# Optimization experiments

Measured on AMD Instinct MI355X. Metric: run time of the kernel, lower is better.

## Reference

```python
import jax, jax.numpy as jnp
import numpy as np

N, S, Z, H, K, DEG = 8192, 4, 64, 128, 4, 16
E = N * DEG


def setup_inputs() -> dict:
    key = jax.random.key(0)
    ks = jax.random.split(key, 9)
    g = lambda k, shape, scale=1.0: jax.random.normal(k, shape, dtype=jnp.float32) * scale
    return dict(
        zIG=g(ks[0], (N, S, Z)),                         # node intention features
        xt_enc=g(ks[1], (N, S, H)),                      # encoded actions per node
        Ws=g(ks[2], (K, H, Z), 1.0 / np.sqrt(Z)),        # attn_s[k] weights (no bias)
        Wd=g(ks[3], (K, H, Z), 1.0 / np.sqrt(Z)),        # attn_d[k] weights
        F2_w1=g(ks[4], (H, 2 * H), 1.0 / np.sqrt(2 * H)),
        F2_w2=g(ks[5], (H, H), 1.0 / np.sqrt(H)),
        F1_w1=g(ks[6], (H, K * H), 1.0 / np.sqrt(K * H)),
        F1_w2=g(ks[7], (H, H), 1.0 / np.sqrt(H)),
        src=jax.random.randint(ks[8], (E,), 0, N),       # random source per edge
        dst=jnp.repeat(jnp.arange(N), DEG),              # regular graph: DEG in-edges per node, grouped
    )


def reference(zIG, xt_enc, Ws, Wd, F2_w1, F2_w2, F1_w1, F1_w2, src, dst):
    n, s, h = xt_enc.shape
    k = Ws.shape[0]
    deg = src.shape[0] // n

    # ---- edge_attention: eIG[e,s,k] = leaky_relu(sum_h (Ws_k z_src)*(Wd_k z_dst)) ----
    zs, zd = zIG[src], zIG[dst]                          # [E,S,Z] irregular gathers
    scores = []
    for kk in range(k):                                  # k is small & structural
        a_s = zs @ Ws[kk].T                              # [E,S,H]
        a_d = zd @ Wd[kk].T                              # [E,S,H]
        scores.append(jax.nn.leaky_relu((a_s * a_d).sum(-1)))  # [E,S]
    eIG = jnp.stack(scores, axis=-1)                     # [E,S,K]

    # ---- message_func: dA = F2(cat(xt_src, xt_dst)) ----
    msg_in = jnp.concatenate([xt_enc[src], xt_enc[dst]], axis=-1)   # [E,S,2H]
    dA = jax.nn.relu(msg_in @ F2_w1.T) @ F2_w2.T                    # [E,S,H]

    # ---- reduce_func: softmax over neighbor mailbox (dim=1), weighted mean ----
    # dst is grouped with constant degree, so the DGL mailbox is a reshape.
    alpha = jax.nn.softmax(eIG.reshape(n, deg, s, k), axis=1)       # [N,D,S,K]
    mail = dA.reshape(n, deg, s, h)                                 # [N,D,S,H]
    res = jnp.einsum('ndsk,ndsh->nskh', alpha, mail) / deg          # mean over D
    res = res.reshape(n, s, k * h)                                  # cat over k (k-major)
    deltax = jax.nn.relu(res @ F1_w1.T) @ F1_w2.T                   # [N,S,H]
    return deltax, alpha
```

## Files before the change

### kernel.cpp

```cpp
#include <hip/hip_runtime.h>
#include <hip/hip_bf16.h>

typedef unsigned short u16;
using ushort8 = __attribute__((ext_vector_type(8))) unsigned short;
using short8  = __attribute__((ext_vector_type(8))) short;
using f32x4   = __attribute__((ext_vector_type(4))) float;

__device__ __forceinline__ float bf2f(u16 v) {
  union { unsigned int u; float f; } x; x.u = ((unsigned int)v) << 16; return x.f;
}
__device__ __forceinline__ u16 f2bf(float f) {
  union { unsigned int u; float f; } x; x.f = f;
  unsigned int r = x.u + 0x7FFFu + ((x.u >> 16) & 1u);
  return (u16)(r >> 16);
}
__device__ __forceinline__ float dot4(float4 a, float4 b) {
  return a.x * b.x + a.y * b.y + a.z * b.z + a.w * b.w;
}
__device__ __forceinline__ void stage_w(const float* g, int stride, int c, u16* Wl, int t) {
  int row = t >> 1, half = t & 1;
  const float4* gp = (const float4*)(g + (size_t)row * stride + c * 64 + half * 32);
  ushort8* d = (ushort8*)(Wl + row * 72 + half * 32);
  #pragma unroll
  for (int i = 0; i < 4; ++i) {
    float4 a = gp[2 * i], b = gp[2 * i + 1];
    ushort8 o;
    o[0] = f2bf(a.x); o[1] = f2bf(a.y); o[2] = f2bf(a.z); o[3] = f2bf(a.w);
    o[4] = f2bf(b.x); o[5] = f2bf(b.y); o[6] = f2bf(b.z); o[7] = f2bf(b.w);
    d[i] = o;
  }
}

__global__ __launch_bounds__(256) void k_mt(const float* __restrict__ Ws,
                                            const float* __restrict__ Wd,
                                            float* __restrict__ MT) {
  int t = blockIdx.x * 256 + threadIdx.x;
  int k = t >> 12, z2 = (t >> 6) & 63, z1 = t & 63;
  const float* wsp = Ws + k * 8192 + z1;
  const float* wdp = Wd + k * 8192 + z2;
  float acc = 0.f;
  #pragma unroll 8
  for (int h = 0; h < 128; ++h) acc += wsp[h * 64] * wdp[h * 64];
  MT[k * 4096 + z2 * 64 + z1] = acc;
}

__global__ __launch_bounds__(256) void k_td(const float* __restrict__ zIG,
                                            const float* __restrict__ MT,
                                            float* __restrict__ td) {
  __shared__ float zf[8 * 256];
  int t = threadIdx.x;
  int nb0 = blockIdx.x * 8;
  {
    const float4* zsrc = (const float4*)(zIG + (size_t)nb0 * 256);
    float4* zd = (float4*)zf;
    zd[t] = zsrc[t];
    zd[t + 256] = zsrc[t + 256];
  }
  __syncthreads();
  int s = t >> 6, k = (t >> 4) & 3, z1q = t & 15;
  const float4* mt4 = (const float4*)MT;
  float4 acc[8];
  #pragma unroll
  for (int g = 0; g < 8; ++g) acc[g] = make_float4(0.f, 0.f, 0.f, 0.f);
  for (int z2 = 0; z2 < 64; ++z2) {
    float4 mv = mt4[k * 1024 + z2 * 16 + z1q];
    #pragma unroll
    for (int g = 0; g < 8; ++g) {
      float zv = zf[g * 256 + s * 64 + z2];
      acc[g].x += mv.x * zv; acc[g].y += mv.y * zv;
      acc[g].z += mv.z * zv; acc[g].w += mv.w * zv;
    }
  }
  int sk = s * 4 + k;
  #pragma unroll
  for (int g = 0; g < 8; ++g)
    *(float4*)&td[(size_t)(nb0 + g) * 1024 + sk * 64 + z1q * 4] = acc[g];
}

__global__ __launch_bounds__(256) void k_ww(const float* __restrict__ F1w1,
                                            const float* __restrict__ F2w2,
                                            float* __restrict__ WW2) {
  int id = blockIdx.x * 256 + threadIdx.x;
  int ho = id >> 9, kk = (id >> 7) & 3, hi = id & 127;
  const float* wa = F1w1 + ho * 512 + kk * 128;
  const float* wb = F2w2 + hi;
  float acc = 0.f;
  #pragma unroll 8
  for (int j = 0; j < 128; ++j) acc += wa[j] * wb[j * 128];
  WW2[ho * 512 + kk * 128 + hi] = acc * 0.0625f;
}

__global__ __launch_bounds__(256) void k_uv(const float* __restrict__ xt,
                                            const float* __restrict__ W1,
                                            u16* __restrict__ u, u16* __restrict__ v) {
  __shared__ u16 Wlu[128 * 72];
  __shared__ u16 Wlv[128 * 72];
  int t = threadIdx.x, lane = t & 63, w = t >> 6;
  size_t rowbase = (size_t)blockIdx.x * 128 + w * 32;
  int l15 = lane & 15, kc = lane >> 4;
  f32x4 au[2][8], av[2][8];
  #pragma unroll
  for (int mt = 0; mt < 2; ++mt)
    #pragma unroll
    for (int nt = 0; nt < 8; ++nt) {
      au[mt][nt] = (f32x4){0.f, 0.f, 0.f, 0.f};
      av[mt][nt] = (f32x4){0.f, 0.f, 0.f, 0.f};
    }
  for (int c = 0; c < 2; ++c) {
    __syncthreads();
    stage_w(W1,       256, c, Wlu, t);
    stage_w(W1 + 128, 256, c, Wlv, t);
    __syncthreads();
    #pragma unroll
    for (int ks = 0; ks < 2; ++ks) {
      short8 af[2];
      #pragma unroll
      for (int mt = 0; mt < 2; ++mt) {
        const float* ap = xt + (rowbase + mt * 16 + l15) * 128 + c * 64 + ks * 32 + kc * 8;
        float4 a0 = *(const float4*)ap, a1 = *(const float4*)(ap + 4);
        u16 tmp[8] = {f2bf(a0.x), f2bf(a0.y), f2bf(a0.z), f2bf(a0.w),
                      f2bf(a1.x), f2bf(a1.y), f2bf(a1.z), f2bf(a1.w)};
        af[mt] = *(short8*)tmp;
      }
      #pragma unroll
      for (int nt = 0; nt < 8; ++nt) {
        short8 bu = *(const short8*)&Wlu[(nt * 16 + l15) * 72 + ks * 32 + kc * 8];
        short8 bv = *(const short8*)&Wlv[(nt * 16 + l15) * 72 + ks * 32 + kc * 8];
        #pragma unroll
        for (int mt = 0; mt < 2; ++mt) {
          au[mt][nt] = __builtin_amdgcn_mfma_f32_16x16x32_bf16(af[mt], bu, au[mt][nt], 0, 0, 0);
          av[mt][nt] = __builtin_amdgcn_mfma_f32_16x16x32_bf16(af[mt], bv, av[mt][nt], 0, 0, 0);
        }
      }
    }
  }
  #pragma unroll
  for (int mt = 0; mt < 2; ++mt)
    #pragma unroll
    for (int nt = 0; nt < 8; ++nt)
      #pragma unroll
      for (int j = 0; j < 4; ++j) {
        size_t idx = (rowbase + mt * 16 + kc * 4 + j) * 128 + nt * 16 + l15;
        u[idx] = f2bf(au[mt][nt][j]);
        v[idx] = f2bf(av[mt][nt][j]);
      }
}

__global__ __launch_bounds__(256) void k_score(
    const float* __restrict__ zIG, const int* __restrict__ src,
    const float* __restrict__ td, const u16* __restrict__ uW, const u16* __restrict__ vW,
    float* __restrict__ out, u16* __restrict__ m_ws) {
  __shared__ int srcIdx[16];
  __shared__ float tds[16 * 68];
  __shared__ float sc[16 * 17];
  __shared__ float al[16 * 17];
  __shared__ float vn[512];

  int t = threadIdx.x, n = blockIdx.x;
  if (t < 16) srcIdx[t] = src[n * 16 + t];
  {
    int r = t >> 4, cc = t & 15;
    *(float4*)&tds[r * 68 + cc * 4] = ((const float4*)(td + (size_t)n * 1024))[r * 16 + cc];
  }
  if (t < 128) ((float4*)vn)[t] = make_float4(bf2f(vW[(size_t)n * 512 + t * 4]),
                                              bf2f(vW[(size_t)n * 512 + t * 4 + 1]),
                                              bf2f(vW[(size_t)n * 512 + t * 4 + 2]),
                                              bf2f(vW[(size_t)n * 512 + t * 4 + 3]));
  __syncthreads();
  {
    int d = t >> 4, s = (t >> 2) & 3, k = t & 3;
    int sn = srcIdx[d];
    const float4* zp = (const float4*)(zIG + (size_t)sn * 256 + s * 64);
    const float4* ta = (const float4*)&tds[(s * 4 + k) * 68];
    float acc = 0.f;
    #pragma unroll
    for (int z4 = 0; z4 < 16; ++z4) acc += dot4(zp[z4], ta[z4]);
    sc[d * 17 + s * 4 + k] = acc > 0.f ? acc : 0.01f * acc;
  }
  __syncthreads();
  {
    int d = t >> 4, sk = t & 15;
    float mx = -3.4e38f;
    #pragma unroll
    for (int dd = 0; dd < 16; ++dd) mx = fmaxf(mx, sc[dd * 17 + sk]);
    float sum = 0.f, eown = 0.f;
    #pragma unroll
    for (int dd = 0; dd < 16; ++dd) {
      float e = __expf(sc[dd * 17 + sk] - mx);
      sum += e;
      if (dd == d) eown = e;
    }
    float a = eown / sum;
    al[d * 17 + sk] = a;
    out[4194304u + (unsigned)n * 256 + t] = a;
  }
  __syncthreads();
  {
    int h = t & 127, s0 = t >> 7;
    float mac[2][4] = {{0.f,0.f,0.f,0.f},{0.f,0.f,0.f,0.f}};
    for (int d = 0; d < 16; ++d) {
      int sn = srcIdx[d];
      #pragma unroll
      for (int pi = 0; pi < 2; ++pi) {
        int s = s0 + pi * 2;
        float uval = bf2f(uW[(size_t)sn * 512 + s * 128 + h]) + vn[s * 128 + h];
        float hid = uval > 0.f ? uval : 0.f;
        #pragma unroll
        for (int k = 0; k < 4; ++k) mac[pi][k] += al[d * 17 + s * 4 + k] * hid;
      }
    }
    #pragma unroll
    for (int pi = 0; pi < 2; ++pi) {
      int s = s0 + pi * 2;
      #pragma unroll
      for (int k = 0; k < 4; ++k)
        m_ws[(size_t)n * 2048 + (s * 4 + k) * 128 + h] = f2bf(mac[pi][k]);
    }
  }
}

__global__ __launch_bounds__(256) void k_fg(const u16* __restrict__ A,
                                            const float* __restrict__ WF,
                                            const float* __restrict__ WG,
                                            float* __restrict__ out) {
  __shared__ u16 Wl[128 * 72];
  __shared__ u16 hidl[128 * 136];
  int t = threadIdx.x, lane = t & 63, w = t >> 6;
  size_t rowbase = (size_t)blockIdx.x * 128 + w * 32;
  int l15 = lane & 15, kc = lane >> 4;
  f32x4 acc[2][8];
  #pragma unroll
  for (int mt = 0; mt < 2; ++mt)
    #pragma unroll
    for (int nt = 0; nt < 8; ++nt) acc[mt][nt] = (f32x4){0.f, 0.f, 0.f, 0.f};
  for (int c = 0; c < 8; ++c) {
    __syncthreads();
    stage_w(WF, 512, c, Wl, t);
    __syncthreads();
    #pragma unroll
    for (int ks = 0; ks < 2; ++ks) {
      short8 af[2];
      #pragma unroll
      for (int mt = 0; mt < 2; ++mt)
        af[mt] = *(const short8*)(A + (rowbase + mt * 16 + l15) * 512 + c * 64 + ks * 32 + kc * 8);
      #pragma unroll
      for (int nt = 0; nt < 8; ++nt) {
        short8 bf = *(const short8*)&Wl[(nt * 16 + l15) * 72 + ks * 32 + kc * 8];
        #pragma unroll
        for (int mt = 0; mt < 2; ++mt)
          acc[mt][nt] = __builtin_amdgcn_mfma_f32_16x16x32_bf16(af[mt], bf, acc[mt][nt], 0, 0, 0);
      }
    }
  }
  #pragma unroll
  for (int mt = 0; mt < 2; ++mt)
    #pragma unroll
    for (int nt = 0; nt < 8; ++nt)
      #pragma unroll
      for (int j = 0; j < 4; ++j)
        hidl[(w * 32 + mt * 16 + kc * 4 + j) * 136 + nt * 16 + l15] =
            f2bf(fmaxf(acc[mt][nt][j], 0.f));
  f32x4 acc2[2][8];
  #pragma unroll
  for (int mt = 0; mt < 2; ++mt)
    #pragma unroll
    for (int nt = 0; nt < 8; ++nt) acc2[mt][nt] = (f32x4){0.f, 0.f, 0.f, 0.f};
  for (int c = 0; c < 2; ++c) {
    __syncthreads();
    stage_w(WG, 128, c, Wl, t);
    __syncthreads();
    #pragma unroll
    for (int ks = 0; ks < 2; ++ks) {
      short8 af[2];
      #pragma unroll
      for (int mt = 0; mt < 2; ++mt)
        af[mt] = *(const short8*)&hidl[(w * 32 + mt * 16 + l15) * 136 + c * 64 + ks * 32 + kc * 8];
      #pragma unroll
      for (int nt = 0; nt < 8; ++nt) {
        short8 bf = *(const short8*)&Wl[(nt * 16 + l15) * 72 + ks * 32 + kc * 8];
        #pragma unroll
        for (int mt = 0; mt < 2; ++mt)
          acc2[mt][nt] = __builtin_amdgcn_mfma_f32_16x16x32_bf16(af[mt], bf, acc2[mt][nt], 0, 0, 0);
      }
    }
  }
  #pragma unroll
  for (int mt = 0; mt < 2; ++mt)
    #pragma unroll
    for (int nt = 0; nt < 8; ++nt)
      #pragma unroll
      for (int j = 0; j < 4; ++j)
        out[(rowbase + mt * 16 + kc * 4 + j) * 128 + nt * 16 + l15] = acc2[mt][nt][j];
}

extern "C" void kernel_launch(void* const* d_in, const int* in_sizes, int n_in,
                              void* d_out, int out_size, void* d_ws, size_t ws_size,
                              hipStream_t stream) {
  const float* zIG  = (const float*)d_in[0];
  const float* xt   = (const float*)d_in[1];
  const float* Ws   = (const float*)d_in[2];
  const float* Wd   = (const float*)d_in[3];
  const float* F2w1 = (const float*)d_in[4];
  const float* F2w2 = (const float*)d_in[5];
  const float* F1w1 = (const float*)d_in[6];
  const float* F1w2 = (const float*)d_in[7];
  const int* src    = (const int*)d_in[8];
  float* out = (float*)d_out;

  char* ws = (char*)d_ws;
  float* MT  = (float*)ws;
  float* td  = (float*)(ws + 65536);
  u16* u     = (u16*)(ws + 65536 + 33554432);
  u16* v     = u + 4194304;
  float* WW2 = (float*)(ws + 50397184);
  u16* m     = (u16*)(ws + 50659328);

  k_mt   <<<64,   256, 0, stream>>>(Ws, Wd, MT);
  k_td   <<<1024, 256, 0, stream>>>(zIG, MT, td);
  k_ww   <<<256,  256, 0, stream>>>(F1w1, F2w2, WW2);
  k_uv   <<<256,  256, 0, stream>>>(xt, F2w1, u, v);
  k_score<<<8192, 256, 0, stream>>>(zIG, src, td, u, v, out, m);
  k_fg   <<<256,  256, 0, stream>>>(m, WW2, F1w2, out);
}
```

Before: 122.5 us.

## Merge independent prep kernels and vectorize score kernel gathers and softmax

Folds k_mt and k_ww into one launch, and k_td and k_uv into a second launch that dispatches on block index, cutting six launches to four and letting independent work overlap. In k_score the per-edge score dot products now have each lane load a quarter of z and reduce through wave shuffles. The softmax is split into separate max/exp and sum phases with an added barrier. The message accumulation reads u and v as packed bf16 pairs, with two h values per thread, and writes packed outputs. These changes aim to cut launch gaps and memory transactions, at the cost of a larger merged kernel with shared-memory use set by its biggest branch, and an extra sync.

```diff
diff --git a/kernel.cpp b/kernel.cpp
--- a/kernel.cpp
+++ b/kernel.cpp
@@ -2,17 +2,24 @@
 #include <hip/hip_bf16.h>
 
 typedef unsigned short u16;
+typedef unsigned int u32;
 using ushort8 = __attribute__((ext_vector_type(8))) unsigned short;
 using short8  = __attribute__((ext_vector_type(8))) short;
 using f32x4   = __attribute__((ext_vector_type(4))) float;
 
 __device__ __forceinline__ float bf2f(u16 v) {
-  union { unsigned int u; float f; } x; x.u = ((unsigned int)v) << 16; return x.f;
+  union { u32 u; float f; } x; x.u = ((u32)v) << 16; return x.f;
+}
+__device__ __forceinline__ float u2f(u32 u) {
+  union { u32 u; float f; } x; x.u = u; return x.f;
 }
 __device__ __forceinline__ u16 f2bf(float f) {
-  union { unsigned int u; float f; } x; x.f = f;
-  unsigned int r = x.u + 0x7FFFu + ((x.u >> 16) & 1u);
+  union { u32 u; float f; } x; x.f = f;
+  u32 r = x.u + 0x7FFFu + ((x.u >> 16) & 1u);
   return (u16)(r >> 16);
+}
+__device__ __forceinline__ u32 pack2bf(float lo, float hi) {
+  return (u32)f2bf(lo) | ((u32)f2bf(hi) << 16);
 }
 __device__ __forceinline__ float dot4(float4 a, float4 b) {
   return a.x * b.x + a.y * b.y + a.z * b.z + a.w * b.w;
@@ -31,119 +38,122 @@
   }
 }
 
-__global__ __launch_bounds__(256) void k_mt(const float* __restrict__ Ws,
-                                            const float* __restrict__ Wd,
-                                            float* __restrict__ MT) {
-  int t = blockIdx.x * 256 + threadIdx.x;
-  int k = t >> 12, z2 = (t >> 6) & 63, z1 = t & 63;
-  const float* wsp = Ws + k * 8192 + z1;
-  const float* wdp = Wd + k * 8192 + z2;
-  float acc = 0.f;
-  #pragma unroll 8
-  for (int h = 0; h < 128; ++h) acc += wsp[h * 64] * wdp[h * 64];
-  MT[k * 4096 + z2 * 64 + z1] = acc;
-}
-
-__global__ __launch_bounds__(256) void k_td(const float* __restrict__ zIG,
-                                            const float* __restrict__ MT,
-                                            float* __restrict__ td) {
-  __shared__ float zf[8 * 256];
+__global__ __launch_bounds__(256) void k_prep(const float* __restrict__ Ws,
+                                              const float* __restrict__ Wd,
+                                              const float* __restrict__ F1w1,
+                                              const float* __restrict__ F2w2,
+                                              float* __restrict__ MT,
+                                              float* __restrict__ WW2) {
+  if (blockIdx.x < 64) {
+    int t = blockIdx.x * 256 + threadIdx.x;
+    int k = t >> 12, z2 = (t >> 6) & 63, z1 = t & 63;
+    const float* wsp = Ws + k * 8192 + z1;
+    const float* wdp = Wd + k * 8192 + z2;
+    float acc = 0.f;
+    #pragma unroll 8
+    for (int h = 0; h < 128; ++h) acc += wsp[h * 64] * wdp[h * 64];
+    MT[k * 4096 + z2 * 64 + z1] = acc;
+  } else {
+    int id = (blockIdx.x - 64) * 256 + threadIdx.x;
+    int ho = id >> 9, kk = (id >> 7) & 3, hi = id & 127;
+    const float* wa = F1w1 + ho * 512 + kk * 128;
+    const float* wb = F2w2 + hi;
+    float acc = 0.f;
+    #pragma unroll 8
+    for (int j = 0; j < 128; ++j) acc += wa[j] * wb[j * 128];
+    WW2[ho * 512 + kk * 128 + hi] = acc * 0.0625f;
+  }
+}
+
+__global__ __launch_bounds__(256) void k_stage2(const float* __restrict__ zIG,
+                                                const float* __restrict__ MT,
+                                                const float* __restrict__ xt,
+                                                const float* __restrict__ W1,
+                                                float* __restrict__ td,
+                                                u16* __restrict__ u, u16* __restrict__ v) {
+  __shared__ __align__(16) char smem[36864];
   int t = threadIdx.x;
-  int nb0 = blockIdx.x * 8;
-  {
-    const float4* zsrc = (const float4*)(zIG + (size_t)nb0 * 256);
-    float4* zd = (float4*)zf;
-    zd[t] = zsrc[t];
-    zd[t + 256] = zsrc[t + 256];
-  }
-  __syncthreads();
-  int s = t >> 6, k = (t >> 4) & 3, z1q = t & 15;
-  const float4* mt4 = (const float4*)MT;
-  float4 acc[8];
-  #pragma unroll
-  for (int g = 0; g < 8; ++g) acc[g] = make_float4(0.f, 0.f, 0.f, 0.f);
-  for (int z2 = 0; z2 < 64; ++z2) {
-    float4 mv = mt4[k * 1024 + z2 * 16 + z1q];
-    #pragma unroll
-    for (int g = 0; g < 8; ++g) {
-      float zv = zf[g * 256 + s * 64 + z2];
-      acc[g].x += mv.x * zv; acc[g].y += mv.y * zv;
-      acc[g].z += mv.z * zv; acc[g].w += mv.w * zv;
-    }
-  }
-  int sk = s * 4 + k;
-  #pragma unroll
-  for (int g = 0; g < 8; ++g)
-    *(float4*)&td[(size_t)(nb0 + g) * 1024 + sk * 64 + z1q * 4] = acc[g];
-}
-
-__global__ __launch_bounds__(256) void k_ww(const float* __restrict__ F1w1,
-                                            const float* __restrict__ F2w2,
-                                            float* __restrict__ WW2) {
-  int id = blockIdx.x * 256 + threadIdx.x;
-  int ho = id >> 9, kk = (id >> 7) & 3, hi = id & 127;
-  const float* wa = F1w1 + ho * 512 + kk * 128;
-  const float* wb = F2w2 + hi;
-  float acc = 0.f;
-  #pragma unroll 8
-  for (int j = 0; j < 128; ++j) acc += wa[j] * wb[j * 128];
-  WW2[ho * 512 + kk * 128 + hi] = acc * 0.0625f;
-}
-
-__global__ __launch_bounds__(256) void k_uv(const float* __restrict__ xt,
-                                            const float* __restrict__ W1,
-                                            u16* __restrict__ u, u16* __restrict__ v) {
-  __shared__ u16 Wlu[128 * 72];
-  __shared__ u16 Wlv[128 * 72];
-  int t = threadIdx.x, lane = t & 63, w = t >> 6;
-  size_t rowbase = (size_t)blockIdx.x * 128 + w * 32;
-  int l15 = lane & 15, kc = lane >> 4;
-  f32x4 au[2][8], av[2][8];
-  #pragma unroll
-  for (int mt = 0; mt < 2; ++mt)
-    #pragma unroll
-    for (int nt = 0; nt < 8; ++nt) {
-      au[mt][nt] = (f32x4){0.f, 0.f, 0.f, 0.f};
-      av[mt][nt] = (f32x4){0.f, 0.f, 0.f, 0.f};
-    }
-  for (int c = 0; c < 2; ++c) {
-    __syncthreads();
-    stage_w(W1,       256, c, Wlu, t);
-    stage_w(W1 + 128, 256, c, Wlv, t);
-    __syncthreads();
-    #pragma unroll
-    for (int ks = 0; ks < 2; ++ks) {
-      short8 af[2];
-      #pragma unroll
-      for (int mt = 0; mt < 2; ++mt) {
-        const float* ap = xt + (rowbase + mt * 16 + l15) * 128 + c * 64 + ks * 32 + kc * 8;
-        float4 a0 = *(const float4*)ap, a1 = *(const float4*)(ap + 4);
-        u16 tmp[8] = {f2bf(a0.x), f2bf(a0.y), f2bf(a0.z), f2bf(a0.w),
-                      f2bf(a1.x), f2bf(a1.y), f2bf(a1.z), f2bf(a1.w)};
-        af[mt] = *(short8*)tmp;
-      }
+  if (blockIdx.x < 1024) {
+    float* zf = (float*)smem;
+    int nb0 = blockIdx.x * 8;
+    {
+      const float4* zsrc = (const float4*)(zIG + (size_t)nb0 * 256);
+      float4* zd = (float4*)zf;
+      zd[t] = zsrc[t];
+      zd[t + 256] = zsrc[t + 256];
+    }
+    __syncthreads();
+    int s = t >> 6, k = (t >> 4) & 3, z1q = t & 15;
+    const float4* mt4 = (const float4*)MT;
+    float4 acc[8];
+    #pragma unroll
+    for (int g = 0; g < 8; ++g) acc[g] = make_float4(0.f, 0.f, 0.f, 0.f);
+    for (int z2 = 0; z2 < 64; ++z2) {
+      float4 mv = mt4[k * 1024 + z2 * 16 + z1q];
+      #pragma unroll
+      for (int g = 0; g < 8; ++g) {
+        float zv = zf[g * 256 + s * 64 + z2];
+        acc[g].x += mv.x * zv; acc[g].y += mv.y * zv;
+        acc[g].z += mv.z * zv; acc[g].w += mv.w * zv;
+      }
+    }
+    int sk = s * 4 + k;
+    #pragma unroll
+    for (int g = 0; g < 8; ++g)
+      *(float4*)&td[(size_t)(nb0 + g) * 1024 + sk * 64 + z1q * 4] = acc[g];
+  } else {
+    u16* Wlu = (u16*)smem;
+    u16* Wlv = (u16*)(smem + 18432);
+    int lane = t & 63, w = t >> 6;
+    size_t rowbase = (size_t)(blockIdx.x - 1024) * 128 + w * 32;
+    int l15 = lane & 15, kc = lane >> 4;
+    f32x4 au[2][8], av[2][8];
+    #pragma unroll
+    for (int mt = 0; mt < 2; ++mt)
       #pragma unroll
       for (int nt = 0; nt < 8; ++nt) {
-        short8 bu = *(const short8*)&Wlu[(nt * 16 + l15) * 72 + ks * 32 + kc * 8];
-        short8 bv = *(const short8*)&Wlv[(nt * 16 + l15) * 72 + ks * 32 + kc * 8];
+        au[mt][nt] = (f32x4){0.f, 0.f, 0.f, 0.f};
+        av[mt][nt] = (f32x4){0.f, 0.f, 0.f, 0.f};
+      }
+    for (int c = 0; c < 2; ++c) {
+      __syncthreads();
+      stage_w(W1,       256, c, Wlu, t);
+      stage_w(W1 + 128, 256, c, Wlv, t);
+      __syncthreads();
+      #pragma unroll
+      for (int ks = 0; ks < 2; ++ks) {
+        short8 af[2];
         #pragma unroll
         for (int mt = 0; mt < 2; ++mt) {
-          au[mt][nt] = __builtin_amdgcn_mfma_f32_16x16x32_bf16(af[mt], bu, au[mt][nt], 0, 0, 0);
-          av[mt][nt] = __builtin_amdgcn_mfma_f32_16x16x32_bf16(af[mt], bv, av[mt][nt], 0, 0, 0);
+          const float* ap = xt + (rowbase + mt * 16 + l15) * 128 + c * 64 + ks * 32 + kc * 8;
+          float4 a0 = *(const float4*)ap, a1 = *(const float4*)(ap + 4);
+          u16 tmp[8] = {f2bf(a0.x), f2bf(a0.y), f2bf(a0.z), f2bf(a0.w),
+                        f2bf(a1.x), f2bf(a1.y), f2bf(a1.z), f2bf(a1.w)};
+          af[mt] = *(short8*)tmp;
         }
-      }
-    }
-  }
-  #pragma unroll
-  for (int mt = 0; mt < 2; ++mt)
-    #pragma unroll
-    for (int nt = 0; nt < 8; ++nt)
-      #pragma unroll
-      for (int j = 0; j < 4; ++j) {
-        size_t idx = (rowbase + mt * 16 + kc * 4 + j) * 128 + nt * 16 + l15;
-        u[idx] = f2bf(au[mt][nt][j]);
-        v[idx] = f2bf(av[mt][nt][j]);
-      }
+        #pragma unroll
+        for (int nt = 0; nt < 8; ++nt) {
+          short8 bu = *(const short8*)&Wlu[(nt * 16 + l15) * 72 + ks * 32 + kc * 8];
+          short8 bv = *(const short8*)&Wlv[(nt * 16 + l15) * 72 + ks * 32 + kc * 8];
+          #pragma unroll
+          for (int mt = 0; mt < 2; ++mt) {
+            au[mt][nt] = __builtin_amdgcn_mfma_f32_16x16x32_bf16(af[mt], bu, au[mt][nt], 0, 0, 0);
+            av[mt][nt] = __builtin_amdgcn_mfma_f32_16x16x32_bf16(af[mt], bv, av[mt][nt], 0, 0, 0);
+          }
+        }
+      }
+    }
+    #pragma unroll
+    for (int mt = 0; mt < 2; ++mt)
+      #pragma unroll
+      for (int nt = 0; nt < 8; ++nt)
+        #pragma unroll
+        for (int j = 0; j < 4; ++j) {
+          size_t idx = (rowbase + mt * 16 + kc * 4 + j) * 128 + nt * 16 + l15;
+          u[idx] = f2bf(au[mt][nt][j]);
+          v[idx] = f2bf(av[mt][nt][j]);
+        }
+  }
 }
 
 __global__ __launch_bounds__(256) void k_score(
@@ -152,9 +162,9 @@
     float* __restrict__ out, u16* __restrict__ m_ws) {
   __shared__ int srcIdx[16];
   __shared__ float tds[16 * 68];
-  __shared__ float sc[16 * 17];
-  __shared__ float al[16 * 17];
-  __shared__ float vn[512];
+  __shared__ float s17[16 * 17];
+  __shared__ float e17[16 * 17];
+  __shared__ float a20[16 * 20];
 
   int t = threadIdx.x, n = blockIdx.x;
   if (t < 16) srcIdx[t] = src[n * 16 + t];
@@ -162,60 +172,72 @@
     int r = t >> 4, cc = t & 15;
     *(float4*)&tds[r * 68 + cc * 4] = ((const float4*)(td + (size_t)n * 1024))[r * 16 + cc];
   }
-  if (t < 128) ((float4*)vn)[t] = make_float4(bf2f(vW[(size_t)n * 512 + t * 4]),
-                                              bf2f(vW[(size_t)n * 512 + t * 4 + 1]),
-                                              bf2f(vW[(size_t)n * 512 + t * 4 + 2]),
-                                              bf2f(vW[(size_t)n * 512 + t * 4 + 3]));
   __syncthreads();
   {
     int d = t >> 4, s = (t >> 2) & 3, k = t & 3;
     int sn = srcIdx[d];
     const float4* zp = (const float4*)(zIG + (size_t)sn * 256 + s * 64);
-    const float4* ta = (const float4*)&tds[(s * 4 + k) * 68];
-    float acc = 0.f;
-    #pragma unroll
-    for (int z4 = 0; z4 < 16; ++z4) acc += dot4(zp[z4], ta[z4]);
-    sc[d * 17 + s * 4 + k] = acc > 0.f ? acc : 0.01f * acc;
+    int base = s * 4;
+    float p0 = 0.f, p1 = 0.f, p2 = 0.f, p3 = 0.f;
+    #pragma unroll
+    for (int i = 0; i < 4; ++i) {
+      float4 zv = zp[i * 4 + k];
+      int o = i * 16 + k * 4;
+      p0 += dot4(zv, *(const float4*)&tds[(base + 0) * 68 + o]);
+      p1 += dot4(zv, *(const float4*)&tds[(base + 1) * 68 + o]);
+      p2 += dot4(zv, *(const float4*)&tds[(base + 2) * 68 + o]);
+      p3 += dot4(zv, *(const float4*)&tds[(base + 3) * 68 + o]);
+    }
+    p0 += __shfl_xor(p0, 1); p1 += __shfl_xor(p1, 1);
+    p2 += __shfl_xor(p2, 1); p3 += __shfl_xor(p3, 1);
+    p0 += __shfl_xor(p0, 2); p1 += __shfl_xor(p1, 2);
+    p2 += __shfl_xor(p2, 2); p3 += __shfl_xor(p3, 2);
+    float acc = (k == 0) ? p0 : (k == 1) ? p1 : (k == 2) ? p2 : p3;
+    s17[d * 17 + base + k] = acc > 0.f ? acc : 0.01f * acc;
   }
   __syncthreads();
-  {
-    int d = t >> 4, sk = t & 15;
+  float e_own;
+  int dC = t >> 4, skC = t & 15;
+  {
     float mx = -3.4e38f;
     #pragma unroll
-    for (int dd = 0; dd < 16; ++dd) mx = fmaxf(mx, sc[dd * 17 + sk]);
-    float sum = 0.f, eown = 0.f;
-    #pragma unroll
-    for (int dd = 0; dd < 16; ++dd) {
-      float e = __expf(sc[dd * 17 + sk] - mx);
-      sum += e;
-      if (dd == d) eown = e;
-    }
-    float a = eown / sum;
-    al[d * 17 + sk] = a;
+    for (int dd = 0; dd < 16; ++dd) mx = fmaxf(mx, s17[dd * 17 + skC]);
+    e_own = __expf(s17[dC * 17 + skC] - mx);
+    e17[dC * 17 + skC] = e_own;
+  }
+  __syncthreads();
+  {
+    float sum = 0.f;
+    #pragma unroll
+    for (int dd = 0; dd < 16; ++dd) sum += e17[dd * 17 + skC];
+    float a = e_own / sum;
+    a20[dC * 20 + skC] = a;
     out[4194304u + (unsigned)n * 256 + t] = a;
   }
   __syncthreads();
   {
-    int h = t & 127, s0 = t >> 7;
-    float mac[2][4] = {{0.f,0.f,0.f,0.f},{0.f,0.f,0.f,0.f}};
+    int hp = t & 63, s = t >> 6;
+    u32 vbits = *(const u32*)(vW + (size_t)n * 512 + s * 128 + hp * 2);
+    float v_lo = u2f(vbits << 16), v_hi = u2f(vbits & 0xffff0000u);
+    const u32* up = (const u32*)uW;
+    float m0l = 0.f, m0h = 0.f, m1l = 0.f, m1h = 0.f;
+    float m2l = 0.f, m2h = 0.f, m3l = 0.f, m3h = 0.f;
     for (int d = 0; d < 16; ++d) {
       int sn = srcIdx[d];
-      #pragma unroll
-      for (int pi = 0; pi < 2; ++pi) {
-        int s = s0 + pi * 2;
-        float uval = bf2f(uW[(size_t)sn * 512 + s * 128 + h]) + vn[s * 128 + h];
-        float hid = uval > 0.f ? uval : 0.f;
-        #pragma unroll
-        for (int k = 0; k < 4; ++k) mac[pi][k] += al[d * 17 + s * 4 + k] * hid;
-      }
-    }
-    #pragma unroll
-    for (int pi = 0; pi < 2; ++pi) {
-      int s = s0 + pi * 2;
-      #pragma unroll
-      for (int k = 0; k < 4; ++k)
-        m_ws[(size_t)n * 2048 + (s * 4 + k) * 128 + h] = f2bf(mac[pi][k]);
-    }
+      u32 ub = up[(size_t)sn * 256 + s * 64 + hp];
+      float r_lo = fmaxf(u2f(ub << 16) + v_lo, 0.f);
+      float r_hi = fmaxf(u2f(ub & 0xffff0000u) + v_hi, 0.f);
+      float4 a = *(const float4*)&a20[d * 20 + s * 4];
+      m0l += a.x * r_lo; m0h += a.x * r_hi;
+      m1l += a.y * r_lo; m1h += a.y * r_hi;
+      m2l += a.z * r_lo; m2h += a.z * r_hi;
+      m3l += a.w * r_lo; m3h += a.w * r_hi;
+    }
+    u32* mp = (u32*)(m_ws + (size_t)n * 2048);
+    mp[(s * 4 + 0) * 64 + hp] = pack2bf(m0l, m0h);
+    mp[(s * 4 + 1) * 64 + hp] = pack2bf(m1l, m1h);
+    mp[(s * 4 + 2) * 64 + hp] = pack2bf(m2l, m2h);
+    mp[(s * 4 + 3) * 64 + hp] = pack2bf(m3l, m3h);
   }
 }
 
@@ -315,10 +337,8 @@
   float* WW2 = (float*)(ws + 50397184);
   u16* m     = (u16*)(ws + 50659328);
 
-  k_mt   <<<64,   256, 0, stream>>>(Ws, Wd, MT);
-  k_td   <<<1024, 256, 0, stream>>>(zIG, MT, td);
-  k_ww   <<<256,  256, 0, stream>>>(F1w1, F2w2, WW2);
-  k_uv   <<<256,  256, 0, stream>>>(xt, F2w1, u, v);
-  k_score<<<8192, 256, 0, stream>>>(zIG, src, td, u, v, out, m);
-  k_fg   <<<256,  256, 0, stream>>>(m, WW2, F1w2, out);
-}
+  k_prep  <<<320,  256, 0, stream>>>(Ws, Wd, F1w1, F2w2, MT, WW2);
+  k_stage2<<<1280, 256, 0, stream>>>(zIG, MT, xt, F2w1, td, u, v);
+  k_score <<<8192, 256, 0, stream>>>(zIG, src, td, u, v, out, m);
+  k_fg    <<<256,  256, 0, stream>>>(m, WW2, F1w2, out);
+}
```

Result: faster. 117.8 us (-3.8%).
